# Kernel optimization log

Measured on AMD Instinct MI355X. Metric: run time of the kernel, lower is better.

Reference implementation:

```python
import jax, jax.numpy as jnp
import numpy as np

B, T, C = 4, 2048, 2048
EPS = 1e-5


def setup_inputs() -> dict:
    key = jax.random.key(0)
    ks = jax.random.split(key, 9)
    s = 1.0 / np.sqrt(C)
    return {
        "x": jax.random.normal(ks[0], (B, T, C), jnp.float32),
        "ln_w": jnp.ones((C,), jnp.float32),
        "ln_b": jnp.zeros((C,), jnp.float32),
        "mix_k": jax.random.uniform(ks[1], (C,), jnp.float32),
        "mix_v": jax.random.uniform(ks[2], (C,), jnp.float32),
        "mix_r": jax.random.uniform(ks[3], (C,), jnp.float32),
        "time_decay": jnp.zeros((C,), jnp.float32),
        "time_first": jnp.zeros((C,), jnp.float32),
        "Wk": jax.random.normal(ks[4], (C, C), jnp.float32) * s,
        "Wv": jax.random.normal(ks[5], (C, C), jnp.float32) * s,
        "Wr": jax.random.normal(ks[6], (C, C), jnp.float32) * s,
        "Wo": jax.random.normal(ks[7], (C, C), jnp.float32) * s,
    }


def reference(x, ln_w, ln_b, mix_k, mix_v, mix_r, time_decay, time_first, Wk, Wv, Wr, Wo):
    # LayerNorm over channel dim
    mu = jnp.mean(x, axis=-1, keepdims=True)
    var = jnp.var(x, axis=-1, keepdims=True)
    xt = (x - mu) * jax.lax.rsqrt(var + EPS) * ln_w + ln_b  # [B,T,C]

    # x_prev at step t is xt at step t-1 (zeros at t=0) -> simple time shift
    prev = jnp.concatenate([jnp.zeros_like(xt[:, :1]), xt[:, :-1]], axis=1)

    # Batched projections (torch Linear: y = x @ W.T)
    k = jnp.einsum('btc,dc->btd', xt * mix_k + prev * (1.0 - mix_k), Wk)
    v = jnp.einsum('btc,dc->btd', xt * mix_v + prev * (1.0 - mix_v), Wv)
    r = jax.nn.sigmoid(jnp.einsum('btc,dc->btd', xt * mix_r + prev * (1.0 - mix_r), Wr))

    decay = jax.nn.sigmoid(time_decay)  # [C]
    first = jnp.exp(time_first)         # [C]

    # Elementwise linear recurrence: state_t = decay * state_{t-1} + k_t
    def step(state, k_t):
        state = state * decay + k_t
        return state, state

    _, states = jax.lax.scan(step, jnp.zeros((B, C), x.dtype), jnp.swapaxes(k, 0, 1))
    state = jnp.swapaxes(states, 0, 1)  # [B,T,C]

    rwkv = (state * first + k) * v
    return jnp.einsum('btc,dc->btd', r * rwkv, Wo)
```

## Files before the change

kernel.cpp:

```cpp
#include <hip/hip_runtime.h>
#include <math.h>

constexpr int B_ = 4;
constexpr int T_ = 2048;
constexpr int C_ = 2048;
constexpr int M_ = B_ * T_;
constexpr float EPS_ = 1e-5f;
constexpr int KSTEPS = C_ / 64;
constexpr int NCH = 32;
constexpr int CHL = T_ / NCH;

typedef __attribute__((ext_vector_type(8))) short short8;
typedef __attribute__((ext_vector_type(4))) float f32x4;

__device__ __forceinline__ unsigned short rne_bf16(float x) {
    unsigned u = __float_as_uint(x);
    unsigned r = u + 0x7FFFu + ((u >> 16) & 1u);
    return (unsigned short)(r >> 16);
}

__global__ __launch_bounds__(256) void ln_mix3_kernel(
        const float* __restrict__ x,
        const float* __restrict__ w,
        const float* __restrict__ bias,
        const float* __restrict__ mxk,
        const float* __restrict__ mxv,
        const float* __restrict__ mxr,
        unsigned short* __restrict__ ak,
        unsigned short* __restrict__ av,
        unsigned short* __restrict__ ar) {
    const int m = blockIdx.x;
    const int tid = threadIdx.x;
    const bool hasPrev = (m & (T_ - 1)) != 0;
    const float* xm = x + (size_t)m * C_;

    float4 a0 = ((const float4*)xm)[tid];
    float4 a1 = ((const float4*)xm)[tid + 256];
    float4 p0 = make_float4(0.f, 0.f, 0.f, 0.f), p1 = p0;
    if (hasPrev) {
        p0 = ((const float4*)(xm - C_))[tid];
        p1 = ((const float4*)(xm - C_))[tid + 256];
    }

    float sm = a0.x + a0.y + a0.z + a0.w + a1.x + a1.y + a1.z + a1.w;
    float qm = a0.x*a0.x + a0.y*a0.y + a0.z*a0.z + a0.w*a0.w
             + a1.x*a1.x + a1.y*a1.y + a1.z*a1.z + a1.w*a1.w;
    float sp = p0.x + p0.y + p0.z + p0.w + p1.x + p1.y + p1.z + p1.w;
    float qp = p0.x*p0.x + p0.y*p0.y + p0.z*p0.z + p0.w*p0.w
             + p1.x*p1.x + p1.y*p1.y + p1.z*p1.z + p1.w*p1.w;

    #pragma unroll
    for (int off = 32; off > 0; off >>= 1) {
        sm += __shfl_down(sm, off, 64);
        qm += __shfl_down(qm, off, 64);
        sp += __shfl_down(sp, off, 64);
        qp += __shfl_down(qp, off, 64);
    }
    __shared__ float red[20];
    const int wid = tid >> 6, lane = tid & 63;
    if (lane == 0) {
        red[wid * 4 + 0] = sm; red[wid * 4 + 1] = qm;
        red[wid * 4 + 2] = sp; red[wid * 4 + 3] = qp;
    }
    __syncthreads();
    if (tid == 0) {
        float tsm = 0.f, tqm = 0.f, tsp = 0.f, tqp = 0.f;
        #pragma unroll
        for (int i = 0; i < 4; ++i) {
            tsm += red[i * 4 + 0]; tqm += red[i * 4 + 1];
            tsp += red[i * 4 + 2]; tqp += red[i * 4 + 3];
        }
        const float mum = tsm / (float)C_;
        const float varm = tqm / (float)C_ - mum * mum;
        const float mup = tsp / (float)C_;
        const float varp = tqp / (float)C_ - mup * mup;
        red[16] = mum; red[17] = rsqrtf(varm + EPS_);
        red[18] = mup; red[19] = rsqrtf(varp + EPS_);
    }
    __syncthreads();
    const float mum = red[16], rsm = red[17];
    const float mup = red[18], rsp = red[19];

    float4 w0 = ((const float4*)w)[tid];
    float4 w1 = ((const float4*)w)[tid + 256];
    float4 b0 = ((const float4*)bias)[tid];
    float4 b1 = ((const float4*)bias)[tid + 256];

    const float avv[8] = {a0.x, a0.y, a0.z, a0.w, a1.x, a1.y, a1.z, a1.w};
    const float pvv[8] = {p0.x, p0.y, p0.z, p0.w, p1.x, p1.y, p1.z, p1.w};
    const float wvv[8] = {w0.x, w0.y, w0.z, w0.w, w1.x, w1.y, w1.z, w1.w};
    const float bvv[8] = {b0.x, b0.y, b0.z, b0.w, b1.x, b1.y, b1.z, b1.w};

    float lm[8], lp[8];
    #pragma unroll
    for (int j = 0; j < 8; ++j) {
        lm[j] = (avv[j] - mum) * rsm * wvv[j] + bvv[j];
        lp[j] = hasPrev ? (pvv[j] - mup) * rsp * wvv[j] + bvv[j] : 0.f;
    }

    const size_t rowbase = (size_t)m * C_;
    auto emit = [&](const float* __restrict__ mx, unsigned short* __restrict__ hi) {
        float4 m0 = ((const float4*)mx)[tid];
        float4 m1 = ((const float4*)mx)[tid + 256];
        const float mm[8] = {m0.x, m0.y, m0.z, m0.w, m1.x, m1.y, m1.z, m1.w};
        ushort4 h[2];
        #pragma unroll
        for (int half = 0; half < 2; ++half) {
            unsigned short hh[4];
            #pragma unroll
            for (int j = 0; j < 4; ++j) {
                const int c = half * 4 + j;
                hh[j] = rne_bf16(lp[c] + (lm[c] - lp[c]) * mm[c]);
            }
            h[half].x = hh[0]; h[half].y = hh[1]; h[half].z = hh[2]; h[half].w = hh[3];
        }
        ((ushort4*)(hi + rowbase))[tid] = h[0];
        ((ushort4*)(hi + rowbase))[tid + 256] = h[1];
    };
    emit(mxk, ak);
    emit(mxv, av);
    emit(mxr, ar);
}

__global__ __launch_bounds__(256) void wconv_kernel(const float* __restrict__ W,
                                                    unsigned short* __restrict__ hi) {
    const int i = blockIdx.x * 256 + threadIdx.x;
    float4 w = ((const float4*)W)[i];
    ushort4 h;
    h.x = rne_bf16(w.x);
    h.y = rne_bf16(w.y);
    h.z = rne_bf16(w.z);
    h.w = rne_bf16(w.w);
    ((ushort4*)hi)[i] = h;
}

template <bool SIG>
__global__ __launch_bounds__(512, 2) void gemm_mfma(const unsigned short* __restrict__ Ahi,
                                                    const unsigned short* __restrict__ Whi,
                                                    float* __restrict__ Y) {
    __shared__ unsigned short lds[2][2][256 * 64];

    const int tid = threadIdx.x;
    const int lane = tid & 63;
    const int wid = tid >> 6;
    const int wr = wid >> 2;
    const int wcn = wid & 3;

    const int bid = blockIdx.x;
    const int swz = (bid & 7) * 32 + (bid >> 3);
    const int m0 = (swz >> 3) * 256;
    const int n0 = (swz & 7) * 256;

    const unsigned short* gA[4];
    const unsigned short* gB[4];
    #pragma unroll
    for (int j = 0; j < 4; ++j) {
        const int ci = j * 512 + tid;
        const int r = ci >> 3, p = ci & 7;
        const int s = p ^ (r & 7);
        gA[j] = Ahi + (size_t)(m0 + r) * C_ + s * 8;
        gB[j] = Whi + (size_t)(n0 + r) * C_ + s * 8;
    }
    const int stage_off = wid * 512;

    const int fr = lane & 15;
    const int kg = lane >> 4;
    const int pS0 = (kg + 0) ^ (fr & 7);
    const int pS1 = (kg + 4) ^ (fr & 7);
    const int baseA0 = (wr * 128 + fr) * 64 + pS0 * 8;
    const int baseA1 = (wr * 128 + fr) * 64 + pS1 * 8;
    const int baseB0 = (wcn * 64 + fr) * 64 + pS0 * 8;
    const int baseB1 = (wcn * 64 + fr) * 64 + pS1 * 8;

    f32x4 acc[8][4] = {};

    auto ISSUE = [&](int buf, int t, int j) {
        const int ko = t * 64;
        __builtin_amdgcn_global_load_lds(
            (const __attribute__((address_space(1))) unsigned int*)(gA[j] + ko),
            (__attribute__((address_space(3))) unsigned int*)&lds[buf][0][j * 4096 + stage_off],
            16, 0, 0);
        __builtin_amdgcn_global_load_lds(
            (const __attribute__((address_space(1))) unsigned int*)(gB[j] + ko),
            (__attribute__((address_space(3))) unsigned int*)&lds[buf][1][j * 4096 + stage_off],
            16, 0, 0);
    };

    auto MFMA_QUAD = [&](int mi0, const short8* a0, const short8* a1,
                         const short8* b0, const short8* b1) {
        #pragma unroll
        for (int ni = 0; ni < 4; ++ni)
            #pragma unroll
            for (int q = 0; q < 4; ++q)
                acc[mi0 + q][ni] = __builtin_amdgcn_mfma_f32_16x16x32_bf16(a0[q], b0[ni], acc[mi0 + q][ni], 0, 0, 0);
        #pragma unroll
        for (int ni = 0; ni < 4; ++ni)
            #pragma unroll
            for (int q = 0; q < 4; ++q)
                acc[mi0 + q][ni] = __builtin_amdgcn_mfma_f32_16x16x32_bf16(a1[q], b1[ni], acc[mi0 + q][ni], 0, 0, 0);
    };

    #pragma unroll
    for (int j = 0; j < 4; ++j) ISSUE(0, 0, j);

    for (int t = 0; t < KSTEPS; ++t) {
        const int cur = t & 1, nxt = cur ^ 1;
        const bool last = (t == KSTEPS - 1);
        const unsigned short* LA = lds[cur][0];
        const unsigned short* LB = lds[cur][1];

        if (!last) {
            #pragma unroll
            for (int j = 0; j < 4; ++j) ISSUE(nxt, t + 1, j);
            asm volatile("s_waitcnt vmcnt(8)" ::: "memory");
        } else {
            asm volatile("s_waitcnt vmcnt(0)" ::: "memory");
        }
        __builtin_amdgcn_s_barrier();

        short8 b0[4], b1[4];
        #pragma unroll
        for (int ni = 0; ni < 4; ++ni) {
            b0[ni] = *(const short8*)&LB[baseB0 + ni * 1024];
            b1[ni] = *(const short8*)&LB[baseB1 + ni * 1024];
        }
        {
            short8 a0[4], a1[4];
            #pragma unroll
            for (int q = 0; q < 4; ++q) {
                a0[q] = *(const short8*)&LA[baseA0 + q * 1024];
                a1[q] = *(const short8*)&LA[baseA1 + q * 1024];
            }
            asm volatile("s_waitcnt lgkmcnt(0)" ::: "memory");
            __builtin_amdgcn_s_setprio(1);
            MFMA_QUAD(0, a0, a1, b0, b1);
            __builtin_amdgcn_s_setprio(0);
        }

        {
            short8 a0[4], a1[4];
            #pragma unroll
            for (int q = 0; q < 4; ++q) {
                a0[q] = *(const short8*)&LA[baseA0 + (4 + q) * 1024];
                a1[q] = *(const short8*)&LA[baseA1 + (4 + q) * 1024];
            }
            asm volatile("s_waitcnt lgkmcnt(0)" ::: "memory");
            __builtin_amdgcn_s_setprio(1);
            MFMA_QUAD(4, a0, a1, b0, b1);
            __builtin_amdgcn_s_setprio(0);
        }

        __builtin_amdgcn_s_barrier();
    }

    const int orow = m0 + wr * 128 + (lane >> 4) * 4;
    const int ocol = n0 + wcn * 64 + fr;
    #pragma unroll
    for (int mi = 0; mi < 8; ++mi)
        #pragma unroll
        for (int ni = 0; ni < 4; ++ni)
            #pragma unroll
            for (int rr = 0; rr < 4; ++rr) {
                float v = acc[mi][ni][rr];
                if (SIG) v = 1.f / (1.f + expf(-v));
                Y[(size_t)(orow + mi * 16 + rr) * C_ + ocol + ni * 16] = v;
            }
}

__global__ __launch_bounds__(256) void wkv_scan1(const float* __restrict__ k,
                                                 const float* __restrict__ time_decay,
                                                 float* __restrict__ chend) {
    const int c0 = (blockIdx.x * 256 + threadIdx.x) * 2;
    const int j = blockIdx.y;
    const int b = blockIdx.z;
    const float2 td = *(const float2*)&time_decay[c0];
    const float d0 = 1.f / (1.f + expf(-td.x));
    const float d1 = 1.f / (1.f + expf(-td.y));
    size_t base = ((size_t)b * T_ + (size_t)j * CHL) * C_ + c0;
    float s0 = 0.f, s1 = 0.f;
    #pragma unroll 8
    for (int t = 0; t < CHL; ++t) {
        const float2 kt = *(const float2*)&k[base];
        s0 = s0 * d0 + kt.x;
        s1 = s1 * d1 + kt.y;
        base += C_;
    }
    *(float2*)&chend[((size_t)b * NCH + j) * C_ + c0] = make_float2(s0, s1);
}

__global__ __launch_bounds__(256) void wkv_scan2(const float* __restrict__ k,
                                                 const float* __restrict__ v,
                                                 const float* __restrict__ r,
                                                 const float* __restrict__ time_decay,
                                                 const float* __restrict__ time_first,
                                                 const float* __restrict__ chend,
                                                 unsigned short* __restrict__ yhi) {
    const int c0 = (blockIdx.x * 256 + threadIdx.x) * 2;
    const int j = blockIdx.y;
    const int b = blockIdx.z;
    const float2 td = *(const float2*)&time_decay[c0];
    const float2 tf = *(const float2*)&time_first[c0];
    const float d0 = 1.f / (1.f + expf(-td.x));
    const float d1 = 1.f / (1.f + expf(-td.y));
    const float f0 = expf(tf.x);
    const float f1 = expf(tf.y);

    float dL0 = d0, dL1 = d1;
    #pragma unroll
    for (int i = 0; i < 6; ++i) { dL0 *= dL0; dL1 *= dL1; }

    float s0 = 0.f, s1 = 0.f;
    for (int i = 0; i < j; ++i) {
        const float2 e = *(const float2*)&chend[((size_t)b * NCH + i) * C_ + c0];
        s0 = s0 * dL0 + e.x;
        s1 = s1 * dL1 + e.y;
    }

    size_t base = ((size_t)b * T_ + (size_t)j * CHL) * C_ + c0;
    #pragma unroll 4
    for (int t = 0; t < CHL; ++t) {
        const float2 kt = *(const float2*)&k[base];
        const float2 vt = *(const float2*)&v[base];
        const float2 rt = *(const float2*)&r[base];
        s0 = s0 * d0 + kt.x;
        s1 = s1 * d1 + kt.y;
        const float y0 = rt.x * ((s0 * f0 + kt.x) * vt.x);
        const float y1 = rt.y * ((s1 * f1 + kt.y) * vt.y);
        ushort2 ph; ph.x = rne_bf16(y0); ph.y = rne_bf16(y1);
        *(ushort2*)&yhi[base] = ph;
        base += C_;
    }
}

extern "C" void kernel_launch(void* const* d_in, const int* in_sizes, int n_in,
                              void* d_out, int out_size, void* d_ws, size_t ws_size,
                              hipStream_t stream) {
    const float* x          = (const float*)d_in[0];
    const float* ln_w       = (const float*)d_in[1];
    const float* ln_b       = (const float*)d_in[2];
    const float* mix_k      = (const float*)d_in[3];
    const float* mix_v      = (const float*)d_in[4];
    const float* mix_r      = (const float*)d_in[5];
    const float* time_decay = (const float*)d_in[6];
    const float* time_first = (const float*)d_in[7];
    const float* Wk         = (const float*)d_in[8];
    const float* Wv         = (const float*)d_in[9];
    const float* Wr         = (const float*)d_in[10];
    const float* Wo         = (const float*)d_in[11];
    float* out = (float*)d_out;

    const size_t planeElems = (size_t)M_ * C_;
    unsigned short* akhi = (unsigned short*)d_ws;
    unsigned short* avhi = akhi + 2 * planeElems;
    unsigned short* arhi = avhi + 2 * planeElems;
    unsigned short* whi  = arhi + 2 * planeElems;

    float* kb = (float*)arhi;
    float* vb = (float*)akhi;
    float* rb = out;
    unsigned short* yhi = avhi;
    float* chend = (float*)whi;

    const int wcBlocks = (C_ * C_ / 4) / 256;
    const dim3 wkvGrid(C_ / 512, NCH, B_);

    ln_mix3_kernel<<<M_, 256, 0, stream>>>(x, ln_w, ln_b, mix_k, mix_v, mix_r,
                                           akhi, avhi, arhi);

    wconv_kernel<<<wcBlocks, 256, 0, stream>>>(Wr, whi);
    gemm_mfma<true><<<256, 512, 0, stream>>>(arhi, whi, rb);

    wconv_kernel<<<wcBlocks, 256, 0, stream>>>(Wk, whi);
    gemm_mfma<false><<<256, 512, 0, stream>>>(akhi, whi, kb);

    wconv_kernel<<<wcBlocks, 256, 0, stream>>>(Wv, whi);
    gemm_mfma<false><<<256, 512, 0, stream>>>(avhi, whi, vb);

    wkv_scan1<<<wkvGrid, 256, 0, stream>>>(kb, time_decay, chend);
    wkv_scan2<<<wkvGrid, 256, 0, stream>>>(kb, vb, rb, time_decay, time_first, chend,
                                           yhi);

    wconv_kernel<<<wcBlocks, 256, 0, stream>>>(Wo, whi);
    gemm_mfma<false><<<256, 512, 0, stream>>>(yhi, whi, out);
}
```

Measured before the change: 400.7 us.

## Interleave next-tile global-to-LDS loads with MFMA pairs in GEMM main loop

The GEMM inner loop now splits each k-step into four phases. Each phase loads two A fragments, issues one quarter of the next tile's global-to-LDS copies, and runs a pair of MFMA groups, with barriers between phases. Previously all next-tile copies were issued up front and waited on with vmcnt(8). The aim is to spread memory traffic across the compute and shrink register pressure from A fragments. The cost is extra barriers per k-step, and the vmcnt(2) wait may stall on the previous tile's final quarter.

```diff
diff --git a/kernel.cpp b/kernel.cpp
--- a/kernel.cpp
+++ b/kernel.cpp
@@ -186,18 +186,19 @@
             16, 0, 0);
     };
 
-    auto MFMA_QUAD = [&](int mi0, const short8* a0, const short8* a1,
+    auto MFMA_PAIR = [&](int mi0, const short8& a0s0, const short8& a0s1,
+                         const short8& a1s0, const short8& a1s1,
                          const short8* b0, const short8* b1) {
         #pragma unroll
-        for (int ni = 0; ni < 4; ++ni)
-            #pragma unroll
-            for (int q = 0; q < 4; ++q)
-                acc[mi0 + q][ni] = __builtin_amdgcn_mfma_f32_16x16x32_bf16(a0[q], b0[ni], acc[mi0 + q][ni], 0, 0, 0);
-        #pragma unroll
-        for (int ni = 0; ni < 4; ++ni)
-            #pragma unroll
-            for (int q = 0; q < 4; ++q)
-                acc[mi0 + q][ni] = __builtin_amdgcn_mfma_f32_16x16x32_bf16(a1[q], b1[ni], acc[mi0 + q][ni], 0, 0, 0);
+        for (int ni = 0; ni < 4; ++ni) {
+            acc[mi0][ni]     = __builtin_amdgcn_mfma_f32_16x16x32_bf16(a0s0, b0[ni], acc[mi0][ni], 0, 0, 0);
+            acc[mi0 + 1][ni] = __builtin_amdgcn_mfma_f32_16x16x32_bf16(a1s0, b0[ni], acc[mi0 + 1][ni], 0, 0, 0);
+        }
+        #pragma unroll
+        for (int ni = 0; ni < 4; ++ni) {
+            acc[mi0][ni]     = __builtin_amdgcn_mfma_f32_16x16x32_bf16(a0s1, b1[ni], acc[mi0][ni], 0, 0, 0);
+            acc[mi0 + 1][ni] = __builtin_amdgcn_mfma_f32_16x16x32_bf16(a1s1, b1[ni], acc[mi0 + 1][ni], 0, 0, 0);
+        }
     };
 
     #pragma unroll
@@ -209,48 +210,47 @@
         const unsigned short* LA = lds[cur][0];
         const unsigned short* LB = lds[cur][1];
 
+        short8 b0[4], b1[4];
+
         if (!last) {
-            #pragma unroll
-            for (int j = 0; j < 4; ++j) ISSUE(nxt, t + 1, j);
-            asm volatile("s_waitcnt vmcnt(8)" ::: "memory");
+            ISSUE(nxt, t + 1, 0);
+            asm volatile("s_waitcnt vmcnt(2)" ::: "memory");
         } else {
             asm volatile("s_waitcnt vmcnt(0)" ::: "memory");
         }
         __builtin_amdgcn_s_barrier();
-
-        short8 b0[4], b1[4];
         #pragma unroll
         for (int ni = 0; ni < 4; ++ni) {
             b0[ni] = *(const short8*)&LB[baseB0 + ni * 1024];
             b1[ni] = *(const short8*)&LB[baseB1 + ni * 1024];
         }
         {
-            short8 a0[4], a1[4];
-            #pragma unroll
-            for (int q = 0; q < 4; ++q) {
-                a0[q] = *(const short8*)&LA[baseA0 + q * 1024];
-                a1[q] = *(const short8*)&LA[baseA1 + q * 1024];
-            }
+            const short8 a0s0 = *(const short8*)&LA[baseA0 + 0 * 1024];
+            const short8 a0s1 = *(const short8*)&LA[baseA1 + 0 * 1024];
+            const short8 a1s0 = *(const short8*)&LA[baseA0 + 1 * 1024];
+            const short8 a1s1 = *(const short8*)&LA[baseA1 + 1 * 1024];
             asm volatile("s_waitcnt lgkmcnt(0)" ::: "memory");
             __builtin_amdgcn_s_setprio(1);
-            MFMA_QUAD(0, a0, a1, b0, b1);
+            MFMA_PAIR(0, a0s0, a0s1, a1s0, a1s1, b0, b1);
             __builtin_amdgcn_s_setprio(0);
         }
-
-        {
-            short8 a0[4], a1[4];
-            #pragma unroll
-            for (int q = 0; q < 4; ++q) {
-                a0[q] = *(const short8*)&LA[baseA0 + (4 + q) * 1024];
-                a1[q] = *(const short8*)&LA[baseA1 + (4 + q) * 1024];
-            }
+        __builtin_amdgcn_s_barrier();
+
+        #pragma unroll
+        for (int p = 1; p < 4; ++p) {
+            const int mi0 = 2 * p;
+            const short8 a0s0 = *(const short8*)&LA[baseA0 + mi0 * 1024];
+            const short8 a0s1 = *(const short8*)&LA[baseA1 + mi0 * 1024];
+            const short8 a1s0 = *(const short8*)&LA[baseA0 + (mi0 + 1) * 1024];
+            const short8 a1s1 = *(const short8*)&LA[baseA1 + (mi0 + 1) * 1024];
+            if (!last) ISSUE(nxt, t + 1, p);
+            __builtin_amdgcn_s_barrier();
             asm volatile("s_waitcnt lgkmcnt(0)" ::: "memory");
             __builtin_amdgcn_s_setprio(1);
-            MFMA_QUAD(4, a0, a1, b0, b1);
+            MFMA_PAIR(mi0, a0s0, a0s1, a1s0, a1s1, b0, b1);
             __builtin_amdgcn_s_setprio(0);
-        }
-
-        __builtin_amdgcn_s_barrier();
+            __builtin_amdgcn_s_barrier();
+        }
     }
 
     const int orow = m0 + wr * 128 + (lane >> 4) * 4;
```

After: 385.1 us. 1.04x faster.
